# Optimization experiments

Hardware: AMD Instinct MI355X
Metric: run time of the kernel (lower is better)

The kernel has to match this reference:

```python
import jax, jax.numpy as jnp
import numpy as np

N = 100000   # nodes
E = 1600000  # edges
F = 128      # node features
H = 64       # hidden_dim
G = 64       # graphs in batch


def setup_inputs() -> dict:
    key = jax.random.key(0)
    ks = jax.random.split(key, 12)
    x = jax.random.normal(ks[0], (N, F), jnp.float32)
    edge_index = jax.random.randint(ks[1], (2, E), 0, N, dtype=jnp.int64)
    batch = jnp.sort(jax.random.randint(ks[2], (N,), 0, G, dtype=jnp.int64))
    s = 0.05
    W1 = jax.random.normal(ks[3], (F, H), jnp.float32) * s
    b1 = jnp.zeros((H,), jnp.float32)
    W2 = jax.random.normal(ks[4], (H, H), jnp.float32) * s
    b2 = jnp.zeros((H,), jnp.float32)
    Wa = jax.random.normal(ks[5], (H, 1), jnp.float32) * s
    ba = jnp.zeros((1,), jnp.float32)
    Wc = jax.random.normal(ks[6], (H, 1), jnp.float32) * s
    bc = jnp.zeros((1,), jnp.float32)
    return {"x": x, "edge_index": edge_index, "batch": batch,
            "W1": W1, "b1": b1, "W2": W2, "b2": b2,
            "Wa": Wa, "ba": ba, "Wc": Wc, "bc": bc}


def _gcn_norm(edge_index, n):
    # Add self-loops, compute symmetric normalization deg^-1/2[src]*deg^-1/2[dst]
    loop = jnp.arange(n, dtype=edge_index.dtype)
    src = jnp.concatenate([edge_index[0], loop])
    dst = jnp.concatenate([edge_index[1], loop])
    deg = jax.ops.segment_sum(jnp.ones_like(src, jnp.float32), dst, num_segments=n)
    dinv = jnp.where(deg > 0, deg ** -0.5, 0.0)
    norm = dinv[src] * dinv[dst]  # [E+N]
    return src, dst, norm


def _gcn_conv(x, W, b, src, dst, norm, n):
    h = x @ W                         # [n, H] dense transform first (PyG order)
    msg = h[src] * norm[:, None]      # gather + normalize [E+n, H]
    agg = jax.ops.segment_sum(msg, dst, num_segments=n)  # scatter-add
    return agg + b


def reference(x, edge_index, batch, W1, b1, W2, b2, Wa, ba, Wc, bc):
    n = x.shape[0]
    src, dst, norm = _gcn_norm(edge_index, n)
    h = jax.nn.relu(_gcn_conv(x, W1, b1, src, dst, norm, n))
    # dropout p=0.1 is identity in eval mode
    h = jax.nn.relu(_gcn_conv(h, W2, b2, src, dst, norm, n))
    action_logits = (h @ Wa + ba)[:, 0]  # [N]
    counts = jax.ops.segment_sum(jnp.ones((n,), jnp.float32), batch, num_segments=G)
    pooled = jax.ops.segment_sum(h, batch, num_segments=G) / jnp.maximum(counts, 1.0)[:, None]
    value = pooled @ Wc + bc  # [G, 1]
    return action_logits, value
```

## Files before the change

### kernel.cpp

```cpp
#include <hip/hip_runtime.h>
#include <hip/hip_fp16.h>
#include <math.h>

#define FEAT 128
#define HID  64
#define BSH  7
#define BNODES (1 << BSH)
#define PB   256
#define SRCM ((1u << 25) - 1)


__global__ void part_hist_k(const int* __restrict__ dst, int* __restrict__ table,
                            int e, int nb) {
    __shared__ int lcnt[1024];
    for (int i = threadIdx.x; i < nb; i += 256) lcnt[i] = 0;
    __syncthreads();
    int eb = (e + PB - 1) / PB;
    int lo = blockIdx.x * eb, hi = min(lo + eb, e);
    for (int i = lo + threadIdx.x; i < hi; i += 256)
        atomicAdd(&lcnt[dst[i] >> BSH], 1);
    __syncthreads();
    for (int k = threadIdx.x; k < nb; k += 256)
        table[k * PB + blockIdx.x] = lcnt[k];
}

__global__ void scan1_k(int* __restrict__ data, int* __restrict__ aux, int L) {
    __shared__ int s[1024];
    int gid = blockIdx.x * 1024 + threadIdx.x;
    int v = (gid < L) ? data[gid] : 0;
    s[threadIdx.x] = v;
    __syncthreads();
    for (int off = 1; off < 1024; off <<= 1) {
        int t = (threadIdx.x >= off) ? s[threadIdx.x - off] : 0;
        __syncthreads();
        s[threadIdx.x] += t;
        __syncthreads();
    }
    if (gid < L) data[gid] = s[threadIdx.x] - v;
    if (threadIdx.x == 1023) aux[blockIdx.x] = s[1023];
}

__global__ void scan2_k(int* aux, int naux) {
    __shared__ int s[1024];
    int v = (threadIdx.x < naux) ? aux[threadIdx.x] : 0;
    s[threadIdx.x] = v;
    __syncthreads();
    for (int off = 1; off < 1024; off <<= 1) {
        int t = (threadIdx.x >= off) ? s[threadIdx.x - off] : 0;
        __syncthreads();
        s[threadIdx.x] += t;
        __syncthreads();
    }
    if (threadIdx.x < naux) aux[threadIdx.x] = s[threadIdx.x] - v;
}

__global__ void part_scatter_k(const int* __restrict__ src, const int* __restrict__ dst,
                               const int* __restrict__ table, const int* __restrict__ aux,
                               unsigned* __restrict__ packed, int e, int nb) {
    __shared__ int loff[1024];
    for (int k = threadIdx.x; k < nb; k += 256) {
        int idx = k * PB + blockIdx.x;
        loff[k] = table[idx] + aux[idx >> 10];
    }
    __syncthreads();
    int eb = (e + PB - 1) / PB;
    int lo = blockIdx.x * eb, hi = min(lo + eb, e);
    for (int i = lo + threadIdx.x; i < hi; i += 256) {
        int d = dst[i];
        int p = atomicAdd(&loff[d >> BSH], 1);
        packed[p] = ((unsigned)(d & (BNODES - 1)) << 25) | (unsigned)src[i];
    }
}


__global__ void bucket_sort_k(const unsigned* __restrict__ packed,
                              const int* __restrict__ table, const int* __restrict__ aux,
                              int* __restrict__ col, int* __restrict__ rowptr,
                              float* __restrict__ dinv, int n, int e, int nb) {
    __shared__ int cnt[BNODES];
    __shared__ int s[BNODES];
    __shared__ int cur[BNODES];
    const int k = blockIdx.x;
    const int t = threadIdx.x;
    if (t < BNODES) cnt[t] = 0;
    __syncthreads();
    int i0 = k * PB;
    int i1 = (k + 1) * PB;
    const int bs = table[i0] + aux[i0 >> 10];
    const int be = (k + 1 < nb) ? (table[i1] + aux[i1 >> 10]) : e;
    for (int i = bs + t; i < be; i += 256)
        atomicAdd(&cnt[packed[i] >> 25], 1);
    __syncthreads();
    if (t < BNODES) s[t] = cnt[t];
    __syncthreads();
    for (int off = 1; off < BNODES; off <<= 1) {
        int v = (t < BNODES && t >= off) ? s[t - off] : 0;
        __syncthreads();
        if (t < BNODES) s[t] += v;
        __syncthreads();
    }
    if (t < BNODES) {
        int base = bs + s[t] - cnt[t];
        cur[t] = base;
        int node = (k << BSH) + t;
        if (node < n) {
            rowptr[node] = base;
            dinv[node] = 1.0f / sqrtf(1.0f + (float)cnt[t]);
            if (node == n - 1) rowptr[n] = base + cnt[t];
        }
    }
    __syncthreads();
    for (int i = bs + t; i < be; i += 256) {
        unsigned u = packed[i];
        int p = atomicAdd(&cur[u >> 25], 1);
        col[p] = (int)(u & SRCM);
    }
}


template<int K>
__global__ __launch_bounds__(256, (K == 128) ? 3 : 4)
void gemm_tile_k(const float* __restrict__ X, const float* __restrict__ W,
                 const float* __restrict__ dinv, __half* __restrict__ out, int n) {
    __shared__ float sX[64][K + 4];
    __shared__ float sW[64][64];
    const int row0 = blockIdx.x * 64;
    const int t  = threadIdx.x;
    const int tx = t & 15;
    const int ty = t >> 4;
    constexpr int KSH = (K == 128) ? 7 : 6;

    const float* xb = X + (size_t)row0 * K;
#pragma unroll
    for (int it = 0; it < K / 16; ++it) {
        int fl = it * 1024 + t * 4;
        int r  = fl >> KSH;
        int k  = fl & (K - 1);
        float4 v = make_float4(0.f, 0.f, 0.f, 0.f);
        if (row0 + r < n) v = *(const float4*)(xb + fl);
        *(float4*)&sX[r][k] = v;
    }

    float acc[4][4] = {};
#pragma unroll
    for (int ph = 0; ph < K / 64; ++ph) {
        __syncthreads();
#pragma unroll
        for (int it = 0; it < 4; ++it) {
            int fl = it * 1024 + t * 4;
            *(float4*)&sW[fl >> 6][fl & 63] = *(const float4*)(W + ph * 64 * HID + fl);
        }
        __syncthreads();

#pragma unroll 8
        for (int k = 0; k < 64; k += 4) {
            float4 a[4], b[4];
#pragma unroll
            for (int i = 0; i < 4; i++) a[i] = *(float4*)&sX[ty * 4 + i][ph * 64 + k];
#pragma unroll
            for (int j = 0; j < 4; j++) b[j] = *(float4*)&sW[k + j][tx * 4];
#pragma unroll
            for (int i = 0; i < 4; i++) {
                acc[i][0] = fmaf(a[i].x, b[0].x, acc[i][0]);
                acc[i][1] = fmaf(a[i].x, b[0].y, acc[i][1]);
                acc[i][2] = fmaf(a[i].x, b[0].z, acc[i][2]);
                acc[i][3] = fmaf(a[i].x, b[0].w, acc[i][3]);
                acc[i][0] = fmaf(a[i].y, b[1].x, acc[i][0]);
                acc[i][1] = fmaf(a[i].y, b[1].y, acc[i][1]);
                acc[i][2] = fmaf(a[i].y, b[1].z, acc[i][2]);
                acc[i][3] = fmaf(a[i].y, b[1].w, acc[i][3]);
                acc[i][0] = fmaf(a[i].z, b[2].x, acc[i][0]);
                acc[i][1] = fmaf(a[i].z, b[2].y, acc[i][1]);
                acc[i][2] = fmaf(a[i].z, b[2].z, acc[i][2]);
                acc[i][3] = fmaf(a[i].z, b[2].w, acc[i][3]);
                acc[i][0] = fmaf(a[i].w, b[3].x, acc[i][0]);
                acc[i][1] = fmaf(a[i].w, b[3].y, acc[i][1]);
                acc[i][2] = fmaf(a[i].w, b[3].z, acc[i][2]);
                acc[i][3] = fmaf(a[i].w, b[3].w, acc[i][3]);
            }
        }
    }

#pragma unroll
    for (int i = 0; i < 4; i++) {
        int gr = row0 + ty * 4 + i;
        if (gr < n) {
            float sc = dinv[gr];
            union { __half2 h[2]; unsigned long long u; } pk;
            pk.h[0] = __floats2half2_rn(acc[i][0] * sc, acc[i][1] * sc);
            pk.h[1] = __floats2half2_rn(acc[i][2] * sc, acc[i][3] * sc);
            *(unsigned long long*)(out + (size_t)gr * HID + tx * 4) = pk.u;
        }
    }
}


template<bool LOGITS>
__global__ void gather_k(const __half* __restrict__ tS, const int* __restrict__ rowptr,
                         const int* __restrict__ col, const float* __restrict__ dinv,
                         const float* __restrict__ b, float* __restrict__ out,
                         const float* __restrict__ Wa, const float* __restrict__ ba,
                         float* __restrict__ logits, int n) {
    int node = (int)((blockIdx.x * (size_t)blockDim.x + threadIdx.x) >> 5);
    int lane = threadIdx.x & 31;
    if (node >= n) return;
    int beg = rowptr[node], end = rowptr[node + 1];
    const __half2* tl = (const __half2*)tS + lane;
    float2 acc = __half22float2(tl[node * 32]);
    int e = beg;
    for (; e + 16 <= end; e += 16) {
        int s[16];
        __half2 v[16];
#pragma unroll
        for (int j = 0; j < 16; j++) s[j] = col[e + j];
#pragma unroll
        for (int j = 0; j < 16; j++) v[j] = tl[s[j] * 32];
        float2 t0 = make_float2(0.f, 0.f), t1 = make_float2(0.f, 0.f);
#pragma unroll
        for (int j = 0; j < 8; j++) {
            float2 f = __half22float2(v[j]);
            t0.x += f.x; t0.y += f.y;
        }
#pragma unroll
        for (int j = 8; j < 16; j++) {
            float2 f = __half22float2(v[j]);
            t1.x += f.x; t1.y += f.y;
        }
        acc.x += t0.x + t1.x;
        acc.y += t0.y + t1.y;
    }
    for (; e + 4 <= end; e += 4) {
        __half2 v0 = tl[col[e] * 32];
        __half2 v1 = tl[col[e + 1] * 32];
        __half2 v2 = tl[col[e + 2] * 32];
        __half2 v3 = tl[col[e + 3] * 32];
        float2 f0 = __half22float2(v0), f1 = __half22float2(v1);
        float2 f2 = __half22float2(v2), f3 = __half22float2(v3);
        acc.x += (f0.x + f1.x) + (f2.x + f3.x);
        acc.y += (f0.y + f1.y) + (f2.y + f3.y);
    }
    for (; e < end; ++e) {
        float2 f = __half22float2(tl[col[e] * 32]);
        acc.x += f.x; acc.y += f.y;
    }
    float d = dinv[node];
    float2 bb = *(const float2*)(b + 2 * lane);
    float h0 = fmaxf(fmaf(d, acc.x, bb.x), 0.0f);
    float h1 = fmaxf(fmaf(d, acc.y, bb.y), 0.0f);
    *(float2*)(out + (size_t)node * HID + 2 * lane) = make_float2(h0, h1);
    if (LOGITS) {
        float2 wa = *(const float2*)(Wa + 2 * lane);
        float p = h0 * wa.x + h1 * wa.y;
#pragma unroll
        for (int off = 16; off > 0; off >>= 1) p += __shfl_down(p, off, 32);
        if (lane == 0) logits[node] = p + ba[0];
    }
}


__global__ void pool_k(const float* __restrict__ h, const int* __restrict__ batch,
                       float* __restrict__ pooled, float* __restrict__ counts, int n) {
    int lane = threadIdx.x & 63;
    int wave = threadIdx.x >> 6;
    int start = blockIdx.x * 256 + wave * 64;
    int end   = min(start + 64, n);
    if (start >= end) return;
    float acc = 0.0f;
    int curg = -1, cnt = 0;
    for (int i = start; i < end; i++) {
        int g = batch[i];
        if (g != curg) {
            if (curg >= 0) {
                atomicAdd(&pooled[curg * HID + lane], acc);
                if (lane == 0) atomicAdd(&counts[curg], (float)cnt);
            }
            curg = g; acc = 0.0f; cnt = 0;
        }
        acc += h[(size_t)i * HID + lane];
        cnt++;
    }
    atomicAdd(&pooled[curg * HID + lane], acc);
    if (lane == 0) atomicAdd(&counts[curg], (float)cnt);
}

__global__ void value_k(const float* __restrict__ pooled, const float* __restrict__ counts,
                        const float* __restrict__ Wc, const float* __restrict__ bc,
                        float* __restrict__ val, int g) {
    int gw   = (int)((blockIdx.x * (size_t)blockDim.x + threadIdx.x) >> 6);
    int lane = threadIdx.x & 63;
    if (gw >= g) return;
    float cnt = fmaxf(counts[gw], 1.0f);
    float p = (pooled[gw * HID + lane] / cnt) * Wc[lane];
#pragma unroll
    for (int off = 32; off > 0; off >>= 1) p += __shfl_down(p, off);
    if (lane == 0) val[gw] = p + bc[0];
}

extern "C" void kernel_launch(void* const* d_in, const int* in_sizes, int n_in,
                              void* d_out, int out_size, void* d_ws, size_t ws_size,
                              hipStream_t stream) {
    const float* x     = (const float*)d_in[0];
    const int*   ei    = (const int*)d_in[1];
    const int*   batch = (const int*)d_in[2];
    const float* W1    = (const float*)d_in[3];
    const float* b1    = (const float*)d_in[4];
    const float* W2    = (const float*)d_in[5];
    const float* b2    = (const float*)d_in[6];
    const float* Wa    = (const float*)d_in[7];
    const float* ba    = (const float*)d_in[8];
    const float* Wc    = (const float*)d_in[9];
    const float* bc    = (const float*)d_in[10];

    const int n = in_sizes[0] / FEAT;
    const int e = in_sizes[1] / 2;
    const int g = out_size - n;
    const int* src = ei;
    const int* dst = ei + e;

    const int nb = (n + BNODES - 1) >> BSH;
    const int L  = nb * PB;

    float*    ws     = (float*)d_ws;
    float*    dinv   = ws;
    float*    bufA   = dinv + n;
    float*    bufB   = bufA + (size_t)n * HID;
    float*    pooled = bufB + (size_t)n * HID;
    float*    counts = pooled + (size_t)g * HID;
    int*      table  = (int*)(counts + g);
    int*      aux    = table + L;
    int*      rowptr = aux + 1024;
    int*      col    = rowptr + n + 1;
    unsigned* packed = (unsigned*)bufA;
    __half*   tS     = (__half*)bufA;

    const int B = 256;
    const int gridT = (n + 63) / 64;
    const int gridG = (int)(((size_t)n * 32 + B - 1) / B);
    const int nb1   = (L + 1023) / 1024;

    hipMemsetAsync(pooled, 0, (size_t)(g * HID + g) * sizeof(float), stream);

    part_hist_k<<<PB, B, 0, stream>>>(dst, table, e, nb);
    scan1_k<<<nb1, 1024, 0, stream>>>(table, aux, L);
    scan2_k<<<1, 1024, 0, stream>>>(aux, nb1);
    part_scatter_k<<<PB, B, 0, stream>>>(src, dst, table, aux, packed, e, nb);
    bucket_sort_k<<<nb, B, 0, stream>>>(packed, table, aux, col, rowptr, dinv, n, e, nb);

    gemm_tile_k<FEAT><<<gridT, B, 0, stream>>>(x, W1, dinv, tS, n);
    gather_k<false><<<gridG, B, 0, stream>>>(tS, rowptr, col, dinv, b1, bufB,
                                             nullptr, nullptr, nullptr, n);

    gemm_tile_k<HID><<<gridT, B, 0, stream>>>(bufB, W2, dinv, tS, n);
    gather_k<true><<<gridG, B, 0, stream>>>(tS, rowptr, col, dinv, b2, bufB,
                                            Wa, ba, (float*)d_out, n);

    pool_k<<<(n + 255) / 256, B, 0, stream>>>(bufB, batch, pooled, counts, n);
    value_k<<<(g * 64 + B - 1) / B, B, 0, stream>>>(pooled, counts, Wc, bc, (float*)d_out + n, g);
}
```

Baseline: 312.2 us.

## Fuse mean pooling into second gather and store layer-1 hidden in fp16

Layer-1 gather now writes its hidden activations as fp16, and the second GEMM reads fp16 input, which halves that intermediate traffic. The second gather no longer writes the final hidden states. It reduces each block's 8 nodes in shared memory and atomically adds them into the pooled sums, which removes the separate pool kernel and the full h write and re-read. Graph counts are now found by binary search over the sorted batch array in value_k. The cost is an extra __syncthreads and atomics in the gather, plus some fp16 rounding of layer-1 outputs.

```diff
diff --git a/kernel.cpp b/kernel.cpp
--- a/kernel.cpp
+++ b/kernel.cpp
@@ -118,9 +118,9 @@
 }
 
 
-template<int K>
+template<int K, bool IN16>
 __global__ __launch_bounds__(256, (K == 128) ? 3 : 4)
-void gemm_tile_k(const float* __restrict__ X, const float* __restrict__ W,
+void gemm_tile_k(const void* __restrict__ Xv, const float* __restrict__ W,
                  const float* __restrict__ dinv, __half* __restrict__ out, int n) {
     __shared__ float sX[64][K + 4];
     __shared__ float sW[64][64];
@@ -130,15 +130,34 @@
     const int ty = t >> 4;
     constexpr int KSH = (K == 128) ? 7 : 6;
 
-    const float* xb = X + (size_t)row0 * K;
-#pragma unroll
-    for (int it = 0; it < K / 16; ++it) {
-        int fl = it * 1024 + t * 4;
-        int r  = fl >> KSH;
-        int k  = fl & (K - 1);
-        float4 v = make_float4(0.f, 0.f, 0.f, 0.f);
-        if (row0 + r < n) v = *(const float4*)(xb + fl);
-        *(float4*)&sX[r][k] = v;
+    if constexpr (!IN16) {
+        const float* xb = (const float*)Xv + (size_t)row0 * K;
+#pragma unroll
+        for (int it = 0; it < K / 16; ++it) {
+            int fl = it * 1024 + t * 4;
+            int r  = fl >> KSH;
+            int k  = fl & (K - 1);
+            float4 v = make_float4(0.f, 0.f, 0.f, 0.f);
+            if (row0 + r < n) v = *(const float4*)(xb + fl);
+            *(float4*)&sX[r][k] = v;
+        }
+    } else {
+        const __half* xb = (const __half*)Xv + (size_t)row0 * K;
+#pragma unroll
+        for (int it = 0; it < K / 32; ++it) {
+            int fl = it * 2048 + t * 8;
+            int r  = fl >> KSH;
+            int k  = fl & (K - 1);
+            float4 raw = make_float4(0.f, 0.f, 0.f, 0.f);
+            if (row0 + r < n) raw = *(const float4*)(xb + fl);
+            const __half2* hp = (const __half2*)&raw;
+#pragma unroll
+            for (int j = 0; j < 4; ++j) {
+                float2 f = __half22float2(hp[j]);
+                sX[r][k + 2 * j]     = f.x;
+                sX[r][k + 2 * j + 1] = f.y;
+            }
+        }
     }
 
     float acc[4][4] = {};
@@ -198,98 +217,110 @@
 template<bool LOGITS>
 __global__ void gather_k(const __half* __restrict__ tS, const int* __restrict__ rowptr,
                          const int* __restrict__ col, const float* __restrict__ dinv,
-                         const float* __restrict__ b, float* __restrict__ out,
+                         const float* __restrict__ b, __half* __restrict__ out,
                          const float* __restrict__ Wa, const float* __restrict__ ba,
-                         float* __restrict__ logits, int n) {
+                         float* __restrict__ logits, const int* __restrict__ batch,
+                         float* __restrict__ pooled, int n) {
+    __shared__ float pga[8][64];
+    __shared__ int   garr[8];
     int node = (int)((blockIdx.x * (size_t)blockDim.x + threadIdx.x) >> 5);
     int lane = threadIdx.x & 31;
-    if (node >= n) return;
-    int beg = rowptr[node], end = rowptr[node + 1];
-    const __half2* tl = (const __half2*)tS + lane;
-    float2 acc = __half22float2(tl[node * 32]);
-    int e = beg;
-    for (; e + 16 <= end; e += 16) {
-        int s[16];
-        __half2 v[16];
-#pragma unroll
-        for (int j = 0; j < 16; j++) s[j] = col[e + j];
-#pragma unroll
-        for (int j = 0; j < 16; j++) v[j] = tl[s[j] * 32];
-        float2 t0 = make_float2(0.f, 0.f), t1 = make_float2(0.f, 0.f);
-#pragma unroll
-        for (int j = 0; j < 8; j++) {
-            float2 f = __half22float2(v[j]);
-            t0.x += f.x; t0.y += f.y;
-        }
-#pragma unroll
-        for (int j = 8; j < 16; j++) {
-            float2 f = __half22float2(v[j]);
-            t1.x += f.x; t1.y += f.y;
-        }
-        acc.x += t0.x + t1.x;
-        acc.y += t0.y + t1.y;
-    }
-    for (; e + 4 <= end; e += 4) {
-        __half2 v0 = tl[col[e] * 32];
-        __half2 v1 = tl[col[e + 1] * 32];
-        __half2 v2 = tl[col[e + 2] * 32];
-        __half2 v3 = tl[col[e + 3] * 32];
-        float2 f0 = __half22float2(v0), f1 = __half22float2(v1);
-        float2 f2 = __half22float2(v2), f3 = __half22float2(v3);
-        acc.x += (f0.x + f1.x) + (f2.x + f3.x);
-        acc.y += (f0.y + f1.y) + (f2.y + f3.y);
-    }
-    for (; e < end; ++e) {
-        float2 f = __half22float2(tl[col[e] * 32]);
-        acc.x += f.x; acc.y += f.y;
-    }
-    float d = dinv[node];
-    float2 bb = *(const float2*)(b + 2 * lane);
-    float h0 = fmaxf(fmaf(d, acc.x, bb.x), 0.0f);
-    float h1 = fmaxf(fmaf(d, acc.y, bb.y), 0.0f);
-    *(float2*)(out + (size_t)node * HID + 2 * lane) = make_float2(h0, h1);
+    int w    = threadIdx.x >> 5;
+    bool active = node < n;
+    if (!LOGITS && !active) return;
+
+    float h0 = 0.f, h1 = 0.f;
+    if (active) {
+        int beg = rowptr[node], end = rowptr[node + 1];
+        const __half2* tl = (const __half2*)tS + lane;
+        float2 acc = __half22float2(tl[node * 32]);
+        int e = beg;
+        for (; e + 16 <= end; e += 16) {
+            int s[16];
+            __half2 v[16];
+#pragma unroll
+            for (int j = 0; j < 16; j++) s[j] = col[e + j];
+#pragma unroll
+            for (int j = 0; j < 16; j++) v[j] = tl[s[j] * 32];
+            float2 t0 = make_float2(0.f, 0.f), t1 = make_float2(0.f, 0.f);
+#pragma unroll
+            for (int j = 0; j < 8; j++) {
+                float2 f = __half22float2(v[j]);
+                t0.x += f.x; t0.y += f.y;
+            }
+#pragma unroll
+            for (int j = 8; j < 16; j++) {
+                float2 f = __half22float2(v[j]);
+                t1.x += f.x; t1.y += f.y;
+            }
+            acc.x += t0.x + t1.x;
+            acc.y += t0.y + t1.y;
+        }
+        for (; e + 4 <= end; e += 4) {
+            __half2 v0 = tl[col[e] * 32];
+            __half2 v1 = tl[col[e + 1] * 32];
+            __half2 v2 = tl[col[e + 2] * 32];
+            __half2 v3 = tl[col[e + 3] * 32];
+            float2 f0 = __half22float2(v0), f1 = __half22float2(v1);
+            float2 f2 = __half22float2(v2), f3 = __half22float2(v3);
+            acc.x += (f0.x + f1.x) + (f2.x + f3.x);
+            acc.y += (f0.y + f1.y) + (f2.y + f3.y);
+        }
+        for (; e < end; ++e) {
+            float2 f = __half22float2(tl[col[e] * 32]);
+            acc.x += f.x; acc.y += f.y;
+        }
+        float d = dinv[node];
+        float2 bb = *(const float2*)(b + 2 * lane);
+        h0 = fmaxf(fmaf(d, acc.x, bb.x), 0.0f);
+        h1 = fmaxf(fmaf(d, acc.y, bb.y), 0.0f);
+        if (!LOGITS) {
+            ((__half2*)out)[node * 32 + lane] = __floats2half2_rn(h0, h1);
+        } else {
+            float2 wa = *(const float2*)(Wa + 2 * lane);
+            float p = h0 * wa.x + h1 * wa.y;
+#pragma unroll
+            for (int off = 16; off > 0; off >>= 1) p += __shfl_down(p, off, 32);
+            if (lane == 0) logits[node] = p + ba[0];
+        }
+    }
+
     if (LOGITS) {
-        float2 wa = *(const float2*)(Wa + 2 * lane);
-        float p = h0 * wa.x + h1 * wa.y;
-#pragma unroll
-        for (int off = 16; off > 0; off >>= 1) p += __shfl_down(p, off, 32);
-        if (lane == 0) logits[node] = p + ba[0];
-    }
-}
-
-
-__global__ void pool_k(const float* __restrict__ h, const int* __restrict__ batch,
-                       float* __restrict__ pooled, float* __restrict__ counts, int n) {
-    int lane = threadIdx.x & 63;
-    int wave = threadIdx.x >> 6;
-    int start = blockIdx.x * 256 + wave * 64;
-    int end   = min(start + 64, n);
-    if (start >= end) return;
-    float acc = 0.0f;
-    int curg = -1, cnt = 0;
-    for (int i = start; i < end; i++) {
-        int g = batch[i];
-        if (g != curg) {
-            if (curg >= 0) {
-                atomicAdd(&pooled[curg * HID + lane], acc);
-                if (lane == 0) atomicAdd(&counts[curg], (float)cnt);
-            }
-            curg = g; acc = 0.0f; cnt = 0;
-        }
-        acc += h[(size_t)i * HID + lane];
-        cnt++;
-    }
-    atomicAdd(&pooled[curg * HID + lane], acc);
-    if (lane == 0) atomicAdd(&counts[curg], (float)cnt);
-}
-
-__global__ void value_k(const float* __restrict__ pooled, const float* __restrict__ counts,
+        *(float2*)&pga[w][2 * lane] = make_float2(active ? h0 : 0.f, active ? h1 : 0.f);
+        if (lane == 0) garr[w] = active ? batch[node] : 0x7fffffff;
+        __syncthreads();
+        int g0 = garr[0];
+        bool uniform = true;
+#pragma unroll
+        for (int i = 1; i < 8; i++) uniform &= (garr[i] == g0 || garr[i] == 0x7fffffff);
+        if (uniform) {
+            if (threadIdx.x < 64) {
+                float s = 0.f;
+#pragma unroll
+                for (int i = 0; i < 8; i++) s += pga[i][threadIdx.x];
+                atomicAdd(&pooled[g0 * HID + threadIdx.x], s);
+            }
+        } else if (active) {
+            int gg = garr[w];
+            atomicAdd(&pooled[gg * HID + 2 * lane], h0);
+            atomicAdd(&pooled[gg * HID + 2 * lane + 1], h1);
+        }
+    }
+}
+
+
+__global__ void value_k(const float* __restrict__ pooled, const int* __restrict__ batch,
                         const float* __restrict__ Wc, const float* __restrict__ bc,
-                        float* __restrict__ val, int g) {
+                        float* __restrict__ val, int n, int g) {
     int gw   = (int)((blockIdx.x * (size_t)blockDim.x + threadIdx.x) >> 6);
     int lane = threadIdx.x & 63;
     if (gw >= g) return;
-    float cnt = fmaxf(counts[gw], 1.0f);
+    int lo = 0, hi = n;
+    while (lo < hi) { int m = (lo + hi) >> 1; if (batch[m] < gw) lo = m + 1; else hi = m; }
+    int b0 = lo;
+    lo = 0; hi = n;
+    while (lo < hi) { int m = (lo + hi) >> 1; if (batch[m] < gw + 1) lo = m + 1; else hi = m; }
+    float cnt = fmaxf((float)(lo - b0), 1.0f);
     float p = (pooled[gw * HID + lane] / cnt) * Wc[lane];
 #pragma unroll
     for (int off = 32; off > 0; off >>= 1) p += __shfl_down(p, off);
@@ -325,20 +356,20 @@
     float*    bufA   = dinv + n;
     float*    bufB   = bufA + (size_t)n * HID;
     float*    pooled = bufB + (size_t)n * HID;
-    float*    counts = pooled + (size_t)g * HID;
-    int*      table  = (int*)(counts + g);
+    int*      table  = (int*)(pooled + (size_t)g * HID);
     int*      aux    = table + L;
     int*      rowptr = aux + 1024;
     int*      col    = rowptr + n + 1;
     unsigned* packed = (unsigned*)bufA;
     __half*   tS     = (__half*)bufA;
+    __half*   h16    = (__half*)bufB;
 
     const int B = 256;
     const int gridT = (n + 63) / 64;
     const int gridG = (int)(((size_t)n * 32 + B - 1) / B);
     const int nb1   = (L + 1023) / 1024;
 
-    hipMemsetAsync(pooled, 0, (size_t)(g * HID + g) * sizeof(float), stream);
+    hipMemsetAsync(pooled, 0, (size_t)g * HID * sizeof(float), stream);
 
     part_hist_k<<<PB, B, 0, stream>>>(dst, table, e, nb);
     scan1_k<<<nb1, 1024, 0, stream>>>(table, aux, L);
@@ -346,14 +377,14 @@
     part_scatter_k<<<PB, B, 0, stream>>>(src, dst, table, aux, packed, e, nb);
     bucket_sort_k<<<nb, B, 0, stream>>>(packed, table, aux, col, rowptr, dinv, n, e, nb);
 
-    gemm_tile_k<FEAT><<<gridT, B, 0, stream>>>(x, W1, dinv, tS, n);
-    gather_k<false><<<gridG, B, 0, stream>>>(tS, rowptr, col, dinv, b1, bufB,
-                                             nullptr, nullptr, nullptr, n);
-
-    gemm_tile_k<HID><<<gridT, B, 0, stream>>>(bufB, W2, dinv, tS, n);
-    gather_k<true><<<gridG, B, 0, stream>>>(tS, rowptr, col, dinv, b2, bufB,
-                                            Wa, ba, (float*)d_out, n);
-
-    pool_k<<<(n + 255) / 256, B, 0, stream>>>(bufB, batch, pooled, counts, n);
-    value_k<<<(g * 64 + B - 1) / B, B, 0, stream>>>(pooled, counts, Wc, bc, (float*)d_out + n, g);
-}
+    gemm_tile_k<FEAT, false><<<gridT, B, 0, stream>>>(x, W1, dinv, tS, n);
+    gather_k<false><<<gridG, B, 0, stream>>>(tS, rowptr, col, dinv, b1, h16,
+                                             nullptr, nullptr, nullptr, nullptr, nullptr, n);
+
+    gemm_tile_k<HID, true><<<gridT, B, 0, stream>>>(h16, W2, dinv, tS, n);
+    gather_k<true><<<gridG, B, 0, stream>>>(tS, rowptr, col, dinv, b2, nullptr,
+                                            Wa, ba, (float*)d_out, batch, pooled, n);
+
+    value_k<<<(g * 64 + B - 1) / B, B, 0, stream>>>(pooled, batch, Wc, bc,
+                                                    (float*)d_out + n, n, g);
+}
```

New measurement: 304.4 us. 1.03x faster.
